# Kernel tuning notes

Measured on AMD Instinct MI355X. Metric: run time of the kernel, lower is better.

## Reference

```python
import jax, jax.numpy as jnp
from jax import lax
import numpy as np

B, CIN, H, W = 32, 256, 56, 56
BOTTLE, GROWTH = 128, 32
EPS = 1e-5
QMAX = 127.0  # 8-bit symmetric


def _fq(x, scale, qmax=QMAX):
    # fake-quantize with straight-through estimator
    q = jnp.clip(jnp.round(x / scale), -qmax - 1.0, qmax) * scale
    return x + lax.stop_gradient(q - x)


def fake_quant_act(x):
    # per-tensor symmetric 8-bit activation quantization (QuantAct)
    scale = lax.stop_gradient(jnp.max(jnp.abs(x)) / QMAX + 1e-8)
    return _fq(x, scale), scale


def quant_weight_pc(w):
    # per-output-channel symmetric 8-bit weight quantization, w: [O,I,kh,kw]
    scale = lax.stop_gradient(jnp.max(jnp.abs(w), axis=(1, 2, 3)) / QMAX + 1e-8)
    return _fq(w, scale[:, None, None, None]), scale


def conv2d(x, w, pad):
    return lax.conv_general_dilated(
        x, w, window_strides=(1, 1), padding=[(pad, pad), (pad, pad)],
        dimension_numbers=("NCHW", "OIHW", "NCHW"))


def setup_inputs() -> dict:
    key = jax.random.key(0)
    ks = jax.random.split(key, 12)
    return {
        "batch": jax.random.normal(ks[0], (B, CIN, H, W), jnp.float32),
        "input_scaling_factor": jnp.float32(0.05),
        "bn1_gamma": jax.random.uniform(ks[1], (CIN,), jnp.float32, 0.5, 1.5),
        "bn1_beta": jax.random.normal(ks[2], (CIN,), jnp.float32) * 0.1,
        "bn1_mean": jax.random.normal(ks[3], (CIN,), jnp.float32) * 0.1,
        "bn1_var": jax.random.uniform(ks[4], (CIN,), jnp.float32, 0.5, 1.5),
        "conv1_w": jax.random.normal(ks[5], (BOTTLE, CIN, 1, 1), jnp.float32) * 0.05,
        "bn2_gamma": jax.random.uniform(ks[6], (BOTTLE,), jnp.float32, 0.5, 1.5),
        "bn2_beta": jax.random.normal(ks[7], (BOTTLE,), jnp.float32) * 0.1,
        "bn2_mean": jax.random.normal(ks[8], (BOTTLE,), jnp.float32) * 0.1,
        "bn2_var": jax.random.uniform(ks[9], (BOTTLE,), jnp.float32, 0.5, 1.5),
        "conv2_w": jax.random.normal(ks[10], (GROWTH, BOTTLE, 3, 3), jnp.float32) * 0.05,
    }


def reference(batch, input_scaling_factor, bn1_gamma, bn1_beta, bn1_mean,
              bn1_var, conv1_w, bn2_gamma, bn2_beta, bn2_mean, bn2_var,
              conv2_w):
    s_in = input_scaling_factor
    # ---- QuantBn1: BN with fake-quantized folded weight/bias ----
    w1 = bn1_gamma * lax.rsqrt(bn1_var + EPS)            # [CIN]
    b1 = bn1_beta - bn1_mean * w1                        # [CIN]
    s_bn = lax.stop_gradient(jnp.max(jnp.abs(w1)) / QMAX + 1e-8)
    w1q = _fq(w1, s_bn)
    b1q = _fq(b1, s_in * s_bn, qmax=2.0 ** 31)           # bias quantized at s_in*s_w
    x = batch * w1q[None, :, None, None] + b1q[None, :, None, None]
    x = jax.nn.relu(x)                                   # act1
    x, s_a1 = fake_quant_act(x)                          # quant_act1
    # ---- QuantBnConv2d: fold bn2 into conv1 (1x1), per-channel weight quant ----
    t = bn2_gamma * lax.rsqrt(bn2_var + EPS)             # [BOTTLE]
    wf = conv1_w * t[:, None, None, None]
    bf = bn2_beta - bn2_mean * t
    wfq, s_w1 = quant_weight_pc(wf)                      # s_w1: [BOTTLE]
    bfq = _fq(bf, s_a1 * s_w1, qmax=2.0 ** 31)
    x = conv2d(x, wfq, pad=0) + bfq[None, :, None, None]
    x = jax.nn.relu(x)                                   # act2
    x, s_a2 = fake_quant_act(x)                          # quant_act2
    # ---- QuantConv2d: 3x3 growth conv, per-channel weight quant ----
    w2q, s_w2 = quant_weight_pc(conv2_w)
    x = conv2d(x, w2q, pad=1)                            # [B, GROWTH, H, W]
    # ---- concat + output requant ----
    cat = jnp.concatenate([batch, x], axis=1)            # [B, CIN+GROWTH, H, W]
    out, s_out = fake_quant_act(cat)                     # quant_act_output
    return out, s_out
```

## Files before the change

### kernel.cpp

```cpp
#include <hip/hip_runtime.h>

typedef __attribute__((ext_vector_type(8))) short bf16x8;
typedef __attribute__((ext_vector_type(4))) float f32x4;

constexpr int B_   = 32;
constexpr int CIN  = 256;
constexpr int HW   = 56 * 56;
constexpr int BOT  = 128;
constexpr int GRW  = 32;
constexpr int COUT = CIN + GRW;
constexpr int NBATCH = B_ * CIN * HW;
constexpr int NOUT   = B_ * COUT * HW;

constexpr int NSLOT = 32;
constexpr int SSTR  = 32;
constexpr int OFF_SLOT = 16;
constexpr int OFF_W1Q  = OFF_SLOT + 4 * NSLOT * SSTR;
constexpr int OFF_B1Q  = OFF_W1Q + 256;
constexpr int OFF_BFQ  = OFF_B1Q + 256;
constexpr int OFF_SC1  = OFF_BFQ + 128;
constexpr int OFF_SC2  = OFF_SC1 + 128;
constexpr int OFF_WQ1B = OFF_SC2 + 32;
constexpr int OFF_W2B  = OFF_WQ1B + 16384;
constexpr int OFF_END  = OFF_W2B + 18432;
constexpr size_t X1Q_BYTE = (size_t)OFF_END * 4;
constexpr size_t X2F_BYTE = X1Q_BYTE + (size_t)NBATCH;
constexpr size_t X2F_FLTS = (size_t)B_ * 58 * 64 * 128;
constexpr size_t X3_BYTE  = X2F_BYTE + X2F_FLTS * 4;

__device__ __forceinline__ void slotAtomicMax(float* ws, int a, int s, float v) {
    atomicMax((unsigned*)ws + OFF_SLOT + a * NSLOT * SSTR + s * SSTR, __float_as_uint(v));
}
__device__ __forceinline__ float slotMax(const float* ws, int a) {
    float m = 0.0f;
    #pragma unroll
    for (int s = 0; s < NSLOT; s++)
        m = fmaxf(m, ws[OFF_SLOT + a * NSLOT * SSTR + s * SSTR]);
    return m;
}

__device__ __forceinline__ float blockReduceMax256(float v) {
    #pragma unroll
    for (int o = 32; o > 0; o >>= 1) v = fmaxf(v, __shfl_down(v, o, 64));
    __shared__ float sm[4];
    if ((threadIdx.x & 63) == 0) sm[threadIdx.x >> 6] = v;
    __syncthreads();
    return fmaxf(fmaxf(sm[0], sm[1]), fmaxf(sm[2], sm[3]));
}
__device__ __forceinline__ float waveReduceMax(float v) {
    #pragma unroll
    for (int o = 32; o > 0; o >>= 1) v = fmaxf(v, __shfl_down(v, o, 64));
    return v;
}
__device__ __forceinline__ float clamp8(float r)   { return fminf(fmaxf(r, -128.0f), 127.0f); }
__device__ __forceinline__ float clampBig(float r) { return fminf(fmaxf(r, -2147483648.0f), 2147483648.0f); }
__device__ __forceinline__ unsigned short bf16u(float f) { return (unsigned short)(__float_as_uint(f) >> 16); }

__global__ void prep1_kernel(const float* __restrict__ g1, const float* __restrict__ b1p,
                             const float* __restrict__ m1, const float* __restrict__ v1,
                             const float* __restrict__ s_in_p, float* __restrict__ ws) {
    int c = threadIdx.x;
    unsigned* scal = (unsigned*)ws;
    for (int s = c; s < OFF_W1Q; s += 256) scal[s] = 0u;
    float s_in = *s_in_p;
    float r = 1.0f / sqrtf(v1[c] + 1e-5f);
    float w1 = __fmul_rn(g1[c], r);
    float b1 = __fsub_rn(b1p[c], __fmul_rn(m1[c], w1));
    float mx = blockReduceMax256(fabsf(w1));
    float s_bn = mx / 127.0f + 1e-8f;
    ws[OFF_W1Q + c] = __fmul_rn(clamp8(rintf(w1 / s_bn)), s_bn);
    float sb = __fmul_rn(s_in, s_bn);
    ws[OFF_B1Q + c] = __fmul_rn(clampBig(rintf(b1 / sb)), sb);
}

__global__ __launch_bounds__(256) void pad0_kernel(float* __restrict__ ws) {
    float4* x2f4 = (float4*)((char*)ws + X2F_BYTE);
    int b = blockIdx.x, t = threadIdx.x;
    float4 z; z.x = z.y = z.z = z.w = 0.0f;
    for (int i = t; i < 2 * 58 * 32; i += 256) {
        int row  = i / (58 * 32);
        int rest = i - row * (58 * 32);
        int slot = rest >> 5, q = rest & 31;
        int hp = row ? 57 : 0;
        x2f4[(((size_t)(b * 58 + hp) * 64 + slot) * 128 >> 2) + q] = z;
    }
    for (int i = t; i < 56 * 2 * 32; i += 256) {
        int hp   = 1 + (i >> 6);
        int rest = i & 63;
        int slot = (rest >> 5) ? 57 : 0;
        int q = rest & 31;
        x2f4[(((size_t)(b * 58 + hp) * 64 + slot) * 128 >> 2) + q] = z;
    }
}

__global__ __launch_bounds__(256) void max1_kernel(const float4* __restrict__ batch4,
                                                   float* __restrict__ ws) {
    const float* w1q = ws + OFF_W1Q;
    const float* b1q = ws + OFF_B1Q;
    int tid = blockIdx.x * 256 + threadIdx.x;
    int row = tid >> 4;
    int f   = tid & 15;
    int c   = row & 255;
    float w = w1q[c], b = b1q[c];
    const float4* p = batch4 + (size_t)row * 784 + f;
    float mx1 = 0.0f, mxb = 0.0f;
    #pragma unroll 7
    for (int k = 0; k < 49; k++) {
        float4 v = p[k * 16];
        float x0 = fmaxf(__fadd_rn(__fmul_rn(v.x, w), b), 0.0f);
        float x1 = fmaxf(__fadd_rn(__fmul_rn(v.y, w), b), 0.0f);
        float x2 = fmaxf(__fadd_rn(__fmul_rn(v.z, w), b), 0.0f);
        float x3 = fmaxf(__fadd_rn(__fmul_rn(v.w, w), b), 0.0f);
        mx1 = fmaxf(mx1, fmaxf(fmaxf(x0, x1), fmaxf(x2, x3)));
        mxb = fmaxf(mxb, fmaxf(fmaxf(fabsf(v.x), fabsf(v.y)), fmaxf(fabsf(v.z), fabsf(v.w))));
    }
    mx1 = blockReduceMax256(mx1);
    __syncthreads();
    mxb = blockReduceMax256(mxb);
    if (threadIdx.x == 0) {
        int s = blockIdx.x & (NSLOT - 1);
        slotAtomicMax(ws, 0, s, mx1);
        slotAtomicMax(ws, 1, s, mxb);
    }
}

__global__ __launch_bounds__(256) void quant1_kernel(const float4* __restrict__ batch4,
                                                     float* __restrict__ ws) {
    __shared__ unsigned ldsq[256 * 17];
    const float* w1q = ws + OFF_W1Q;
    const float* b1q = ws + OFF_B1Q;
    float s_a1 = slotMax(ws, 0) / 127.0f + 1e-8f;
    int b = blockIdx.x / 49, hw0 = (blockIdx.x % 49) * 64;
    int t = threadIdx.x;
    int f = t & 15, cb = t >> 4;
    #pragma unroll
    for (int j = 0; j < 16; j++) {
        int c = cb + j * 16;
        float w = w1q[c], bb = b1q[c];
        float4 v = batch4[(b * 256 + c) * 784 + (hw0 >> 2) + f];
        unsigned q0 = (unsigned)(int)clamp8(rintf(fmaxf(__fadd_rn(__fmul_rn(v.x, w), bb), 0.0f) / s_a1));
        unsigned q1 = (unsigned)(int)clamp8(rintf(fmaxf(__fadd_rn(__fmul_rn(v.y, w), bb), 0.0f) / s_a1));
        unsigned q2 = (unsigned)(int)clamp8(rintf(fmaxf(__fadd_rn(__fmul_rn(v.z, w), bb), 0.0f) / s_a1));
        unsigned q3 = (unsigned)(int)clamp8(rintf(fmaxf(__fadd_rn(__fmul_rn(v.w, w), bb), 0.0f) / s_a1));
        ldsq[c * 17 + f] = q0 | (q1 << 8) | (q2 << 16) | (q3 << 24);
    }
    __syncthreads();
    const unsigned char* l8 = (const unsigned char*)ldsq;
    uint4* outv = (uint4*)((char*)ws + X1Q_BYTE);
    int hwl = t >> 2, cq = (t & 3) * 16;
    #pragma unroll
    for (int k = 0; k < 4; k++) {
        int c0 = cq + k * 64;
        unsigned u[4] = {0u, 0u, 0u, 0u};
        #pragma unroll
        for (int i = 0; i < 16; i++) {
            unsigned by = l8[(c0 + i) * 68 + hwl];
            u[i >> 2] |= by << ((i & 3) * 8);
        }
        uint4 val; val.x = u[0]; val.y = u[1]; val.z = u[2]; val.w = u[3];
        outv[(((size_t)b * 3136 + hw0 + hwl) * 256 + c0) >> 4] = val;
    }
}

__global__ void prep2_kernel(const float* __restrict__ c1w,
                             const float* __restrict__ g2, const float* __restrict__ b2,
                             const float* __restrict__ m2, const float* __restrict__ v2,
                             const float* __restrict__ c2w, float* __restrict__ ws) {
    int bi = blockIdx.x;
    int t = threadIdx.x;
    unsigned short* wq1b = (unsigned short*)(ws + OFF_WQ1B);
    unsigned short* w2b  = (unsigned short*)(ws + OFF_W2B);
    if (bi < BOT) {
        int o = bi;
        float tt = __fmul_rn(g2[o], 1.0f / sqrtf(v2[o] + 1e-5f));
        float wf = __fmul_rn(c1w[o * CIN + t], tt);
        float mx = blockReduceMax256(fabsf(wf));
        float s_w1 = mx / 127.0f + 1e-8f;
        float m = clamp8(rintf(wf / s_w1));
        wq1b[o * CIN + t] = bf16u(m);
        if (t == 0) {
            float s_a1 = slotMax(ws, 0) / 127.0f + 1e-8f;
            ws[OFF_SC1 + o] = __fmul_rn(s_a1, s_w1);
            float bf = __fsub_rn(b2[o], __fmul_rn(m2[o], tt));
            float sb = __fmul_rn(s_a1, s_w1);
            ws[OFF_BFQ + o] = __fmul_rn(clampBig(rintf(bf / sb)), sb);
        }
    } else {
        int g = bi - BOT;
        float mx = 0.0f;
        for (int s = t; s < BOT * 9; s += 256) mx = fmaxf(mx, fabsf(c2w[g * BOT * 9 + s]));
        mx = blockReduceMax256(mx);
        float s_w2 = mx / 127.0f + 1e-8f;
        for (int s = t; s < BOT * 9; s += 256) {
            int c = s / 9, tap = s - c * 9;
            float m = clamp8(rintf(c2w[g * BOT * 9 + s] / s_w2));
            w2b[(tap * GRW + g) * BOT + c] = bf16u(m);
        }
        if (t == 0) ws[OFF_SC2 + g] = s_w2;
    }
}

__global__ __launch_bounds__(256) void conv1_kernel(float* __restrict__ ws) {
    __shared__ unsigned short lA[64 * 136];
    __shared__ unsigned short lW[128 * 136];
    __shared__ float wred[4];
    const unsigned char* x1q = (const unsigned char*)((char*)ws + X1Q_BYTE);
    const unsigned short* wq1b = (const unsigned short*)(ws + OFF_WQ1B);
    const float* sc1 = ws + OFF_SC1;
    const float* bfq = ws + OFF_BFQ;
    float* x2f = (float*)((char*)ws + X2F_BYTE);
    int b = blockIdx.x / 49, hw0 = (blockIdx.x % 49) * 64;
    int t = threadIdx.x, lane = t & 63, wv = t >> 6;
    int quad = lane >> 4, l16 = lane & 15;
    int mhalf = wv & 1, nhalf = wv >> 1;
    f32x4 acc[2][4];
    #pragma unroll
    for (int i = 0; i < 2; i++)
        #pragma unroll
        for (int j = 0; j < 4; j++) acc[i][j] = (f32x4){0.f, 0.f, 0.f, 0.f};

    for (int kc = 0; kc < 256; kc += 128) {
        __syncthreads();
        {
            int cb = t & 7, hwi = t >> 3;
            #pragma unroll
            for (int r = 0; r < 2; r++) {
                int hw = hwi + r * 32;
                uint4 p = *(const uint4*)(x1q + ((size_t)b * 3136 + hw0 + hw) * 256 + kc + cb * 16);
                unsigned wd[4] = {p.x, p.y, p.z, p.w};
                bf16x8 t0, t1;
                #pragma unroll
                for (int j = 0; j < 8; j++)
                    t0[j] = (short)bf16u((float)((wd[j >> 2] >> ((j & 3) * 8)) & 255u));
                #pragma unroll
                for (int j = 0; j < 8; j++)
                    t1[j] = (short)bf16u((float)((wd[2 + (j >> 2)] >> ((j & 3) * 8)) & 255u));
                *(bf16x8*)&lA[hw * 136 + cb * 16] = t0;
                *(bf16x8*)&lA[hw * 136 + cb * 16 + 8] = t1;
            }
        }
        {
            int cb = t & 7, oi = t >> 3;
            #pragma unroll
            for (int r = 0; r < 4; r++) {
                int o = oi + r * 32;
                uint4 p0 = *(const uint4*)(wq1b + o * 256 + kc + cb * 16);
                uint4 p1 = *(const uint4*)(wq1b + o * 256 + kc + cb * 16 + 8);
                *(uint4*)&lW[o * 136 + cb * 16] = p0;
                *(uint4*)&lW[o * 136 + cb * 16 + 8] = p1;
            }
        }
        __syncthreads();
        #pragma unroll
        for (int ks = 0; ks < 4; ks++) {
            bf16x8 a0 = *(const bf16x8*)&lA[(mhalf * 32 + l16) * 136 + ks * 32 + quad * 8];
            bf16x8 a1 = *(const bf16x8*)&lA[(mhalf * 32 + 16 + l16) * 136 + ks * 32 + quad * 8];
            #pragma unroll
            for (int nt = 0; nt < 4; nt++) {
                bf16x8 bfr = *(const bf16x8*)&lW[(nhalf * 64 + nt * 16 + l16) * 136 + ks * 32 + quad * 8];
                acc[0][nt] = __builtin_amdgcn_mfma_f32_16x16x32_bf16(a0, bfr, acc[0][nt], 0, 0, 0);
                acc[1][nt] = __builtin_amdgcn_mfma_f32_16x16x32_bf16(a1, bfr, acc[1][nt], 0, 0, 0);
            }
        }
    }
    float mx = 0.0f;
    #pragma unroll
    for (int mt = 0; mt < 2; mt++) {
        int hwg = hw0 + mhalf * 32 + mt * 16 + quad * 4;
        int h = (int)(((unsigned)hwg * 9363u) >> 19);
        int w = hwg - h * 56;
        float* base0 = x2f + ((size_t)(b * 58 + h + 1) * 64 + (w + 1)) * 128;
        #pragma unroll
        for (int nt = 0; nt < 4; nt++) {
            int o = nhalf * 64 + nt * 16 + l16;
            float s = sc1[o], bb = bfq[o];
            float v0 = fmaxf(__fadd_rn(__fmul_rn(acc[mt][nt][0], s), bb), 0.0f);
            float v1 = fmaxf(__fadd_rn(__fmul_rn(acc[mt][nt][1], s), bb), 0.0f);
            float v2 = fmaxf(__fadd_rn(__fmul_rn(acc[mt][nt][2], s), bb), 0.0f);
            float v3 = fmaxf(__fadd_rn(__fmul_rn(acc[mt][nt][3], s), bb), 0.0f);
            mx = fmaxf(mx, fmaxf(fmaxf(v0, v1), fmaxf(v2, v3)));
            base0[o]       = v0;
            base0[o + 128] = v1;
            base0[o + 256] = v2;
            base0[o + 384] = v3;
        }
    }
    mx = waveReduceMax(mx);
    if (lane == 0) wred[wv] = mx;
    __syncthreads();
    if (t == 0) {
        float m = fmaxf(fmaxf(wred[0], wred[1]), fmaxf(wred[2], wred[3]));
        slotAtomicMax(ws, 2, blockIdx.x & (NSLOT - 1), m);
    }
}

__global__ __launch_bounds__(256) void conv2_kernel(float* __restrict__ ws) {
    __shared__ unsigned short xt[4 * 58 * 40];
    __shared__ unsigned short wt[9 * 32 * 40];
    __shared__ float wred[4];
    const float* x2f = (const float*)((char*)ws + X2F_BYTE);
    const unsigned short* w2b = (const unsigned short*)(ws + OFF_W2B);
    const float* sc2 = ws + OFF_SC2;
    float* x3 = (float*)((char*)ws + X3_BYTE);
    int b = blockIdx.x / 28, hg = blockIdx.x % 28;
    int t = threadIdx.x, lane = t & 63, wv = t >> 6;
    int quad = lane >> 4, l16 = lane & 15;
    int r = wv >> 1;
    int h = hg * 2 + r;
    int wq = wv & 1;
    int w0 = wq * 24;
    float s_a2 = slotMax(ws, 2) / 127.0f + 1e-8f;
    float rinv = 1.0f / s_a2;
    const float* src = x2f + (size_t)(b * 58 + hg * 2) * 64 * 128;

    f32x4 acc[2][2];
    #pragma unroll
    for (int i = 0; i < 2; i++) { acc[i][0] = (f32x4){0.f,0.f,0.f,0.f}; acc[i][1] = (f32x4){0.f,0.f,0.f,0.f}; }

    for (int cs = 0; cs < 4; cs++) {
        __syncthreads();
        for (int s = t; s < 1152; s += 256) {
            int gi = s >> 2, q = s & 3;
            *(uint4*)&wt[gi * 40 + q * 8] = *(const uint4*)(w2b + gi * 128 + cs * 32 + q * 8);
        }
        #pragma unroll
        for (int k = 0; k < 8; k++) {
            int idx = t + k * 256;
            if (idx < 1856) {
                int row = idx / 464;
                int rem = idx - row * 464;
                int slot = rem >> 3, c4 = rem & 7;
                f32x4 v = *(const f32x4*)(src + (size_t)(row * 64 + slot) * 128 + cs * 32 + c4 * 4);
                unsigned q0 = bf16u(clamp8(rintf(v[0] * rinv)));
                unsigned q1 = bf16u(clamp8(rintf(v[1] * rinv)));
                unsigned q2 = bf16u(clamp8(rintf(v[2] * rinv)));
                unsigned q3 = bf16u(clamp8(rintf(v[3] * rinv)));
                uint2 pk; pk.x = q0 | (q1 << 16); pk.y = q2 | (q3 << 16);
                *(uint2*)&xt[(row * 58 + slot) * 40 + c4 * 4] = pk;
            }
        }
        __syncthreads();
        #pragma unroll
        for (int tap = 0; tap < 9; tap++) {
            int dh = tap / 3, dw = tap % 3;
            bf16x8 b0 = *(const bf16x8*)&wt[(tap * 32 + l16) * 40 + quad * 8];
            bf16x8 b1 = *(const bf16x8*)&wt[(tap * 32 + 16 + l16) * 40 + quad * 8];
            #pragma unroll
            for (int mt = 0; mt < 2; mt++) {
                int slot = w0 + mt * 16 + l16 + dw;
                bf16x8 a = *(const bf16x8*)&xt[((r + dh) * 58 + slot) * 40 + quad * 8];
                acc[mt][0] = __builtin_amdgcn_mfma_f32_16x16x32_bf16(a, b0, acc[mt][0], 0, 0, 0);
                acc[mt][1] = __builtin_amdgcn_mfma_f32_16x16x32_bf16(a, b1, acc[mt][1], 0, 0, 0);
            }
        }
    }
    float mx = 0.0f;
    #pragma unroll
    for (int nt = 0; nt < 2; nt++) {
        int g = nt * 16 + l16;
        float s2 = __fmul_rn(s_a2, sc2[g]);
        #pragma unroll
        for (int mt = 0; mt < 2; mt++) {
            int wb = w0 + mt * 16 + quad * 4;
            if (wq == 0 || wb >= 32) {
                float4 v;
                v.x = __fmul_rn(acc[mt][nt][0], s2);
                v.y = __fmul_rn(acc[mt][nt][1], s2);
                v.z = __fmul_rn(acc[mt][nt][2], s2);
                v.w = __fmul_rn(acc[mt][nt][3], s2);
                mx = fmaxf(mx, fmaxf(fmaxf(fabsf(v.x), fabsf(v.y)), fmaxf(fabsf(v.z), fabsf(v.w))));
                *(float4*)&x3[(size_t)(b * GRW + g) * HW + h * 56 + wb] = v;
            }
        }
    }
    mx = waveReduceMax(mx);
    if (lane == 0) wred[wv] = mx;
    __syncthreads();
    if (t == 0) {
        float m = fmaxf(fmaxf(wred[0], wred[1]), fmaxf(wred[2], wred[3]));
        slotAtomicMax(ws, 3, blockIdx.x & (NSLOT - 1), m);
    }
}

__global__ __launch_bounds__(256) void outq_kernel(const float4* __restrict__ batch4,
                                                   const float* __restrict__ ws,
                                                   float* __restrict__ out) {
    const float4* x34 = (const float4*)((const char*)ws + X3_BYTE);
    float maxb = slotMax(ws, 1);
    float max3 = slotMax(ws, 3);
    float s_out = fmaxf(maxb, max3) / 127.0f + 1e-8f;
    float4* out4 = (float4*)out;
    int n4 = NOUT / 4;
    for (int i = blockIdx.x * blockDim.x + threadIdx.x; i < n4; i += gridDim.x * blockDim.x) {
        int chl = i / 784;
        int b = chl / COUT;
        int ch = chl - b * COUT;
        int hw4 = i - chl * 784;
        float4 v;
        if (ch < CIN) v = batch4[(b * CIN + ch) * 784 + hw4];
        else          v = x34[(b * GRW + (ch - CIN)) * 784 + hw4];
        float4 r;
        r.x = __fmul_rn(clamp8(rintf(v.x / s_out)), s_out);
        r.y = __fmul_rn(clamp8(rintf(v.y / s_out)), s_out);
        r.z = __fmul_rn(clamp8(rintf(v.z / s_out)), s_out);
        r.w = __fmul_rn(clamp8(rintf(v.w / s_out)), s_out);
        out4[i] = r;
    }
    if (blockIdx.x == 0 && threadIdx.x == 0) out[NOUT] = s_out;
}

extern "C" void kernel_launch(void* const* d_in, const int* in_sizes, int n_in,
                              void* d_out, int out_size, void* d_ws, size_t ws_size,
                              hipStream_t stream) {
    const float* batch = (const float*)d_in[0];
    const float* s_in  = (const float*)d_in[1];
    const float* g1    = (const float*)d_in[2];
    const float* b1    = (const float*)d_in[3];
    const float* m1    = (const float*)d_in[4];
    const float* v1    = (const float*)d_in[5];
    const float* c1w   = (const float*)d_in[6];
    const float* g2    = (const float*)d_in[7];
    const float* b2    = (const float*)d_in[8];
    const float* m2    = (const float*)d_in[9];
    const float* v2    = (const float*)d_in[10];
    const float* c2w   = (const float*)d_in[11];
    float* out = (float*)d_out;
    float* ws  = (float*)d_ws;

    hipLaunchKernelGGL(prep1_kernel, dim3(1), dim3(256), 0, stream, g1, b1, m1, v1, s_in, ws);
    hipLaunchKernelGGL(pad0_kernel, dim3(32), dim3(256), 0, stream, ws);
    hipLaunchKernelGGL(max1_kernel, dim3(512), dim3(256), 0, stream, (const float4*)batch, ws);
    hipLaunchKernelGGL(quant1_kernel, dim3(32 * 49), dim3(256), 0, stream, (const float4*)batch, ws);
    hipLaunchKernelGGL(prep2_kernel, dim3(160), dim3(256), 0, stream, c1w, g2, b2, m2, v2, c2w, ws);
    hipLaunchKernelGGL(conv1_kernel, dim3(32 * 49), dim3(256), 0, stream, ws);
    hipLaunchKernelGGL(conv2_kernel, dim3(32 * 28), dim3(256), 0, stream, ws);
    hipLaunchKernelGGL(outq_kernel, dim3(4096), dim3(256), 0, stream, (const float4*)batch, ws, out);
}
```

Measured before the change: 334.5 us.

## Fuse BN1 activation quantization into conv1 and merge prep/pad kernels

The activation quantization (BN1, ReLU, 8-bit quant) moves from a separate quant1 kernel into conv1. conv1 now reads the fp32 batch directly, quantizes to bf16 values and transposes them through shared memory into the MFMA A-tile. This removes the int8 intermediate tensor write/read and one launch, and prep1 and pad0 are merged into one kernel. In exchange conv1 uses more LDS and gains an extra sync and transpose pass, which may lower occupancy.

```diff
diff --git a/kernel.cpp b/kernel.cpp
--- a/kernel.cpp
+++ b/kernel.cpp
@@ -23,8 +23,7 @@
 constexpr int OFF_WQ1B = OFF_SC2 + 32;
 constexpr int OFF_W2B  = OFF_WQ1B + 16384;
 constexpr int OFF_END  = OFF_W2B + 18432;
-constexpr size_t X1Q_BYTE = (size_t)OFF_END * 4;
-constexpr size_t X2F_BYTE = X1Q_BYTE + (size_t)NBATCH;
+constexpr size_t X2F_BYTE = (size_t)OFF_END * 4;
 constexpr size_t X2F_FLTS = (size_t)B_ * 58 * 64 * 128;
 constexpr size_t X3_BYTE  = X2F_BYTE + X2F_FLTS * 4;
 
@@ -56,26 +55,27 @@
 __device__ __forceinline__ float clampBig(float r) { return fminf(fmaxf(r, -2147483648.0f), 2147483648.0f); }
 __device__ __forceinline__ unsigned short bf16u(float f) { return (unsigned short)(__float_as_uint(f) >> 16); }
 
-__global__ void prep1_kernel(const float* __restrict__ g1, const float* __restrict__ b1p,
-                             const float* __restrict__ m1, const float* __restrict__ v1,
-                             const float* __restrict__ s_in_p, float* __restrict__ ws) {
-    int c = threadIdx.x;
-    unsigned* scal = (unsigned*)ws;
-    for (int s = c; s < OFF_W1Q; s += 256) scal[s] = 0u;
-    float s_in = *s_in_p;
-    float r = 1.0f / sqrtf(v1[c] + 1e-5f);
-    float w1 = __fmul_rn(g1[c], r);
-    float b1 = __fsub_rn(b1p[c], __fmul_rn(m1[c], w1));
-    float mx = blockReduceMax256(fabsf(w1));
-    float s_bn = mx / 127.0f + 1e-8f;
-    ws[OFF_W1Q + c] = __fmul_rn(clamp8(rintf(w1 / s_bn)), s_bn);
-    float sb = __fmul_rn(s_in, s_bn);
-    ws[OFF_B1Q + c] = __fmul_rn(clampBig(rintf(b1 / sb)), sb);
-}
-
-__global__ __launch_bounds__(256) void pad0_kernel(float* __restrict__ ws) {
+__global__ __launch_bounds__(256) void prep_kernel(const float* __restrict__ g1, const float* __restrict__ b1p,
+                                                   const float* __restrict__ m1, const float* __restrict__ v1,
+                                                   const float* __restrict__ s_in_p, float* __restrict__ ws) {
+    int t = threadIdx.x;
+    if (blockIdx.x == 0) {
+        int c = t;
+        unsigned* scal = (unsigned*)ws;
+        for (int s = c; s < OFF_W1Q; s += 256) scal[s] = 0u;
+        float s_in = *s_in_p;
+        float r = 1.0f / sqrtf(v1[c] + 1e-5f);
+        float w1 = __fmul_rn(g1[c], r);
+        float b1 = __fsub_rn(b1p[c], __fmul_rn(m1[c], w1));
+        float mx = blockReduceMax256(fabsf(w1));
+        float s_bn = mx / 127.0f + 1e-8f;
+        ws[OFF_W1Q + c] = __fmul_rn(clamp8(rintf(w1 / s_bn)), s_bn);
+        float sb = __fmul_rn(s_in, s_bn);
+        ws[OFF_B1Q + c] = __fmul_rn(clampBig(rintf(b1 / sb)), sb);
+        return;
+    }
+    int b = blockIdx.x - 1;
     float4* x2f4 = (float4*)((char*)ws + X2F_BYTE);
-    int b = blockIdx.x, t = threadIdx.x;
     float4 z; z.x = z.y = z.z = z.w = 0.0f;
     for (int i = t; i < 2 * 58 * 32; i += 256) {
         int row  = i / (58 * 32);
@@ -121,44 +121,6 @@
         int s = blockIdx.x & (NSLOT - 1);
         slotAtomicMax(ws, 0, s, mx1);
         slotAtomicMax(ws, 1, s, mxb);
-    }
-}
-
-__global__ __launch_bounds__(256) void quant1_kernel(const float4* __restrict__ batch4,
-                                                     float* __restrict__ ws) {
-    __shared__ unsigned ldsq[256 * 17];
-    const float* w1q = ws + OFF_W1Q;
-    const float* b1q = ws + OFF_B1Q;
-    float s_a1 = slotMax(ws, 0) / 127.0f + 1e-8f;
-    int b = blockIdx.x / 49, hw0 = (blockIdx.x % 49) * 64;
-    int t = threadIdx.x;
-    int f = t & 15, cb = t >> 4;
-    #pragma unroll
-    for (int j = 0; j < 16; j++) {
-        int c = cb + j * 16;
-        float w = w1q[c], bb = b1q[c];
-        float4 v = batch4[(b * 256 + c) * 784 + (hw0 >> 2) + f];
-        unsigned q0 = (unsigned)(int)clamp8(rintf(fmaxf(__fadd_rn(__fmul_rn(v.x, w), bb), 0.0f) / s_a1));
-        unsigned q1 = (unsigned)(int)clamp8(rintf(fmaxf(__fadd_rn(__fmul_rn(v.y, w), bb), 0.0f) / s_a1));
-        unsigned q2 = (unsigned)(int)clamp8(rintf(fmaxf(__fadd_rn(__fmul_rn(v.z, w), bb), 0.0f) / s_a1));
-        unsigned q3 = (unsigned)(int)clamp8(rintf(fmaxf(__fadd_rn(__fmul_rn(v.w, w), bb), 0.0f) / s_a1));
-        ldsq[c * 17 + f] = q0 | (q1 << 8) | (q2 << 16) | (q3 << 24);
-    }
-    __syncthreads();
-    const unsigned char* l8 = (const unsigned char*)ldsq;
-    uint4* outv = (uint4*)((char*)ws + X1Q_BYTE);
-    int hwl = t >> 2, cq = (t & 3) * 16;
-    #pragma unroll
-    for (int k = 0; k < 4; k++) {
-        int c0 = cq + k * 64;
-        unsigned u[4] = {0u, 0u, 0u, 0u};
-        #pragma unroll
-        for (int i = 0; i < 16; i++) {
-            unsigned by = l8[(c0 + i) * 68 + hwl];
-            u[i >> 2] |= by << ((i & 3) * 8);
-        }
-        uint4 val; val.x = u[0]; val.y = u[1]; val.z = u[2]; val.w = u[3];
-        outv[(((size_t)b * 3136 + hw0 + hwl) * 256 + c0) >> 4] = val;
     }
 }
 
@@ -200,19 +162,24 @@
     }
 }
 
-__global__ __launch_bounds__(256) void conv1_kernel(float* __restrict__ ws) {
+__global__ __launch_bounds__(256) void conv1_kernel(const float4* __restrict__ batch4,
+                                                    float* __restrict__ ws) {
+    __shared__ unsigned ls[128 * 33];
     __shared__ unsigned short lA[64 * 136];
     __shared__ unsigned short lW[128 * 136];
     __shared__ float wred[4];
-    const unsigned char* x1q = (const unsigned char*)((char*)ws + X1Q_BYTE);
     const unsigned short* wq1b = (const unsigned short*)(ws + OFF_WQ1B);
+    const float* w1q = ws + OFF_W1Q;
+    const float* b1q = ws + OFF_B1Q;
     const float* sc1 = ws + OFF_SC1;
     const float* bfq = ws + OFF_BFQ;
     float* x2f = (float*)((char*)ws + X2F_BYTE);
+    float s_a1 = slotMax(ws, 0) / 127.0f + 1e-8f;
     int b = blockIdx.x / 49, hw0 = (blockIdx.x % 49) * 64;
     int t = threadIdx.x, lane = t & 63, wv = t >> 6;
     int quad = lane >> 4, l16 = lane & 15;
     int mhalf = wv & 1, nhalf = wv >> 1;
+    int f = t & 15, cb = t >> 4;
     f32x4 acc[2][4];
     #pragma unroll
     for (int i = 0; i < 2; i++)
@@ -222,32 +189,53 @@
     for (int kc = 0; kc < 256; kc += 128) {
         __syncthreads();
         {
-            int cb = t & 7, hwi = t >> 3;
             #pragma unroll
-            for (int r = 0; r < 2; r++) {
-                int hw = hwi + r * 32;
-                uint4 p = *(const uint4*)(x1q + ((size_t)b * 3136 + hw0 + hw) * 256 + kc + cb * 16);
-                unsigned wd[4] = {p.x, p.y, p.z, p.w};
-                bf16x8 t0, t1;
-                #pragma unroll
-                for (int j = 0; j < 8; j++)
-                    t0[j] = (short)bf16u((float)((wd[j >> 2] >> ((j & 3) * 8)) & 255u));
-                #pragma unroll
-                for (int j = 0; j < 8; j++)
-                    t1[j] = (short)bf16u((float)((wd[2 + (j >> 2)] >> ((j & 3) * 8)) & 255u));
-                *(bf16x8*)&lA[hw * 136 + cb * 16] = t0;
-                *(bf16x8*)&lA[hw * 136 + cb * 16 + 8] = t1;
+            for (int j = 0; j < 8; j++) {
+                int cl = cb + j * 16;
+                int c  = kc + cl;
+                float w = w1q[c], bb = b1q[c];
+                float4 v = batch4[(size_t)(b * 256 + c) * 784 + (hw0 >> 2) + f];
+                unsigned q0 = bf16u(clamp8(rintf(fmaxf(__fadd_rn(__fmul_rn(v.x, w), bb), 0.0f) / s_a1)));
+                unsigned q1 = bf16u(clamp8(rintf(fmaxf(__fadd_rn(__fmul_rn(v.y, w), bb), 0.0f) / s_a1)));
+                unsigned q2 = bf16u(clamp8(rintf(fmaxf(__fadd_rn(__fmul_rn(v.z, w), bb), 0.0f) / s_a1)));
+                unsigned q3 = bf16u(clamp8(rintf(fmaxf(__fadd_rn(__fmul_rn(v.w, w), bb), 0.0f) / s_a1)));
+                ls[cl * 33 + f * 2]     = q0 | (q1 << 16);
+                ls[cl * 33 + f * 2 + 1] = q2 | (q3 << 16);
             }
         }
         {
-            int cb = t & 7, oi = t >> 3;
+            int cw = t & 7, oi = t >> 3;
             #pragma unroll
             for (int r = 0; r < 4; r++) {
                 int o = oi + r * 32;
-                uint4 p0 = *(const uint4*)(wq1b + o * 256 + kc + cb * 16);
-                uint4 p1 = *(const uint4*)(wq1b + o * 256 + kc + cb * 16 + 8);
-                *(uint4*)&lW[o * 136 + cb * 16] = p0;
-                *(uint4*)&lW[o * 136 + cb * 16 + 8] = p1;
+                uint4 p0 = *(const uint4*)(wq1b + o * 256 + kc + cw * 16);
+                uint4 p1 = *(const uint4*)(wq1b + o * 256 + kc + cw * 16 + 8);
+                *(uint4*)&lW[o * 136 + cw * 16] = p0;
+                *(uint4*)&lW[o * 136 + cw * 16 + 8] = p1;
+            }
+        }
+        __syncthreads();
+        {
+            #pragma unroll
+            for (int k = 0; k < 4; k++) {
+                int task = t + k * 256;
+                int hw = task & 63, c8 = task >> 6;
+                int base = (hw >> 2) * 2 + ((hw >> 1) & 1);
+                int sh = (hw & 1) * 16;
+                unsigned v0 = ls[(c8 * 8 + 0) * 33 + base] >> sh;
+                unsigned v1 = ls[(c8 * 8 + 1) * 33 + base] >> sh;
+                unsigned v2 = ls[(c8 * 8 + 2) * 33 + base] >> sh;
+                unsigned v3 = ls[(c8 * 8 + 3) * 33 + base] >> sh;
+                unsigned v4 = ls[(c8 * 8 + 4) * 33 + base] >> sh;
+                unsigned v5 = ls[(c8 * 8 + 5) * 33 + base] >> sh;
+                unsigned v6 = ls[(c8 * 8 + 6) * 33 + base] >> sh;
+                unsigned v7 = ls[(c8 * 8 + 7) * 33 + base] >> sh;
+                uint4 pk;
+                pk.x = (v0 & 0xffffu) | (v1 << 16);
+                pk.y = (v2 & 0xffffu) | (v3 << 16);
+                pk.z = (v4 & 0xffffu) | (v5 << 16);
+                pk.w = (v6 & 0xffffu) | (v7 << 16);
+                *(uint4*)&lA[hw * 136 + c8 * 8] = pk;
             }
         }
         __syncthreads();
@@ -427,12 +415,10 @@
     float* out = (float*)d_out;
     float* ws  = (float*)d_ws;
 
-    hipLaunchKernelGGL(prep1_kernel, dim3(1), dim3(256), 0, stream, g1, b1, m1, v1, s_in, ws);
-    hipLaunchKernelGGL(pad0_kernel, dim3(32), dim3(256), 0, stream, ws);
+    hipLaunchKernelGGL(prep_kernel, dim3(33), dim3(256), 0, stream, g1, b1, m1, v1, s_in, ws);
     hipLaunchKernelGGL(max1_kernel, dim3(512), dim3(256), 0, stream, (const float4*)batch, ws);
-    hipLaunchKernelGGL(quant1_kernel, dim3(32 * 49), dim3(256), 0, stream, (const float4*)batch, ws);
     hipLaunchKernelGGL(prep2_kernel, dim3(160), dim3(256), 0, stream, c1w, g2, b2, m2, v2, c2w, ws);
-    hipLaunchKernelGGL(conv1_kernel, dim3(32 * 49), dim3(256), 0, stream, ws);
+    hipLaunchKernelGGL(conv1_kernel, dim3(32 * 49), dim3(256), 0, stream, (const float4*)batch, ws);
     hipLaunchKernelGGL(conv2_kernel, dim3(32 * 28), dim3(256), 0, stream, ws);
     hipLaunchKernelGGL(outq_kernel, dim3(4096), dim3(256), 0, stream, (const float4*)batch, ws, out);
 }
```

Result: slower. 346.3 us (+3.5%).
